# Kernel optimization log

Measured on AMD Instinct MI355X. Metric: run time of the kernel, lower is better.

Reference implementation:

```python
import jax, jax.numpy as jnp
import numpy as np

B, T, H = 256, 512, 1024


def setup_inputs() -> dict:
    key = jax.random.key(0)
    ks = jax.random.split(key, 11)
    s = 1.0 / np.sqrt(H)
    u = lambda k, shape: jax.random.uniform(k, shape, jnp.float32, -s, s)
    return {
        "x": jax.random.normal(ks[0], (B, T), jnp.float32),
        "W_ih1": u(ks[1], (4 * H, 1)),
        "W_hh1": u(ks[2], (4 * H, H)),
        "b_ih1": u(ks[3], (4 * H,)),
        "b_hh1": u(ks[4], (4 * H,)),
        "W_ih2": u(ks[5], (4 * H, H)),
        "W_hh2": u(ks[6], (4 * H, H)),
        "b_ih2": u(ks[7], (4 * H,)),
        "b_hh2": u(ks[8], (4 * H,)),
        "W_out": u(ks[9], (1, H)),
        "b_out": u(ks[10], (1,)),
        "future": 0,
    }


def _lstm_cell(x, h, c, W_ih, W_hh, b):
    # PyTorch LSTMCell gate order: i, f, g, o
    gates = x @ W_ih.T + h @ W_hh.T + b
    i, f, g, o = jnp.split(gates, 4, axis=-1)
    c_new = jax.nn.sigmoid(f) * c + jax.nn.sigmoid(i) * jnp.tanh(g)
    h_new = jax.nn.sigmoid(o) * jnp.tanh(c_new)
    return h_new, c_new


def reference(x, W_ih1, W_hh1, b_ih1, b_hh1, W_ih2, W_hh2, b_ih2, b_hh2, W_out, b_out, future):
    Bn = x.shape[0]
    Hd = W_hh1.shape[1]
    b1 = b_ih1 + b_hh1
    b2 = b_ih2 + b_hh2

    def step(carry, x_t):
        h1, c1, h2, c2 = carry
        h1, c1 = _lstm_cell(x_t, h1, c1, W_ih1, W_hh1, b1)
        h2, c2 = _lstm_cell(h1, h2, c2, W_ih2, W_hh2, b2)
        out = h2 @ W_out.T + b_out  # [B, 1]
        return (h1, c1, h2, c2), out

    xs = x.T[:, :, None]  # [T, B, 1]
    carry0 = tuple(jnp.zeros((Bn, Hd), x.dtype) for _ in range(4))
    carry, outs = jax.lax.scan(step, carry0, xs)  # outs: [T, B, 1]
    outputs = [outs[:, :, 0].T]  # [B, T]

    # closed-loop future prediction (future is a static Python int)
    out = outs[-1]
    for _ in range(future):
        carry, out = step(carry, out)
        outputs.append(out)
    return jnp.concatenate(outputs, axis=1)
```

## Files before the change

### kernel.cpp

```cpp
#include <hip/hip_runtime.h>
#include <hip/hip_cooperative_groups.h>
#include <math.h>

namespace cg = cooperative_groups;

#define Bsz 256
#define Tsz 512
#define GSTR 258

using half8 = __attribute__((ext_vector_type(8))) _Float16;
using half4 = __attribute__((ext_vector_type(4))) _Float16;
using f32x4 = __attribute__((ext_vector_type(4))) float;

#define MFMA_V(acc, a, b) (acc) = __builtin_amdgcn_mfma_f32_16x16x32_f16((a), (b), (acc), 0, 0, 0)
#define INV2048 (1.0f / 2048.0f)

__device__ __forceinline__ float sigm(float v)   { return 1.0f / (1.0f + expf(-v)); }
__device__ __forceinline__ float tanh_f(float v) { float e = expf(2.0f * v); return 1.0f - 2.0f / (e + 1.0f); }

__device__ __forceinline__ void split8(const float* p, half8& hi, half8& lo) {
    float4 v0 = *(const float4*)p, v1 = *(const float4*)(p + 4);
    float vv[8] = {v0.x, v0.y, v0.z, v0.w, v1.x, v1.y, v1.z, v1.w};
    #pragma unroll
    for (int j = 0; j < 8; ++j) {
        hi[j] = (_Float16)vv[j];
        lo[j] = (_Float16)((vv[j] - (float)hi[j]) * 2048.0f);
    }
}

__device__ __forceinline__ void step_barrier(unsigned* bar0, unsigned* bar1,
                                             unsigned* phase2, unsigned* dummyv,
                                             int bx, int isLead, unsigned xcc,
                                             unsigned nLead, unsigned it1) {
    __syncthreads();
    if (threadIdx.x == 0) {
        unsigned old = __hip_atomic_fetch_add(&bar0[(bx & 15) << 5], 1u,
                                              __ATOMIC_RELAXED, __HIP_MEMORY_SCOPE_AGENT);
        if ((old & 15u) == 15u)
            __hip_atomic_fetch_add(bar1, 1u, __ATOMIC_RELAXED, __HIP_MEMORY_SCOPE_AGENT);
        if (isLead) {
            while (__hip_atomic_load(bar1, __ATOMIC_RELAXED, __HIP_MEMORY_SCOPE_AGENT) < 16u * it1)
                __builtin_amdgcn_s_sleep(1);
            __hip_atomic_fetch_add(&dummyv[xcc << 5], 1u,
                                   __ATOMIC_ACQ_REL, __HIP_MEMORY_SCOPE_AGENT);
            __hip_atomic_fetch_add(phase2, 1u,
                                   __ATOMIC_RELAXED, __HIP_MEMORY_SCOPE_AGENT);
        }
        while (__hip_atomic_load(phase2, __ATOMIC_RELAXED, __HIP_MEMORY_SCOPE_AGENT) < nLead * it1)
            __builtin_amdgcn_s_sleep(1);
        asm volatile("buffer_inv sc0" ::: "memory");
    }
    __syncthreads();
}

__global__ __launch_bounds__(512, 1) void lstm_persist(
    const float* __restrict__ x,
    const float* __restrict__ W_ih1, const float* __restrict__ W_hh1,
    const float* __restrict__ b_ih1, const float* __restrict__ b_hh1,
    const float* __restrict__ W_ih2, const float* __restrict__ W_hh2,
    const float* __restrict__ b_ih2, const float* __restrict__ b_hh2,
    const float* __restrict__ W_out, const float* __restrict__ b_out,
    float* __restrict__ out, char* __restrict__ ws)
{
    __shared__ float gAcc[32 * GSTR];
    __shared__ float poArr[2 * GSTR];
    __shared__ float bp[32], wihp[32], woutp[8];
    __shared__ float bouts_s;
    __shared__ unsigned isLead_s, xcc_s, nLead_s;

    cg::grid_group grid = cg::this_grid();

    const int tid  = threadIdx.x;
    const int lane = tid & 63;
    const int wv   = tid >> 6;
    const int m    = lane & 15;
    const int quad = lane >> 4;
    const int bx   = blockIdx.x;
    const bool isL2 = (bx >= 128);
    const int rg   = isL2 ? (bx - 128) : bx;
    const int HO   = rg << 3;

    float*    xT       = (float*)ws;
    _Float16* hswz     = (_Float16*)(ws + (512 << 10));
    float*    partials = (float*)(ws + (512 << 10) + (4 << 20));
    unsigned* bar0     = (unsigned*)(ws + (512 << 10) + (4 << 20) + (256 << 10));
    unsigned* bar1     = bar0 + 1024;
    unsigned* phase2   = bar0 + 1056;
    unsigned* nLeadCt  = bar0 + 1057;
    unsigned* claimA   = bar0 + 1088;
    unsigned* dummyv   = bar0 + 1536;

    #define HBUF(p, l, hl) (hswz + ((((p) << 2) | ((l) << 1) | (hl)) << 18))

    if (bx == 0)
        for (int i = tid; i < 2048; i += 512) bar0[i] = 0u;
    if (tid < 32) {
        const int row = ((tid & 3) << 10) + HO + (tid >> 2);
        if (!isL2) {
            bp[tid]   = b_ih1[row] + b_hh1[row];
            wihp[tid] = W_ih1[row];
        } else {
            bp[tid] = b_ih2[row] + b_hh2[row];
            if (tid < 8) woutp[tid] = W_out[HO + tid];
        }
        if (tid == 0) bouts_s = b_out[0];
    }
    {
        const int gidx = bx * 512 + tid;
        *(float4*)((char*)hswz + (2u << 20) + (size_t)gidx * 16) = make_float4(0, 0, 0, 0);
        xT[gidx] = x[(gidx & 255) * Tsz + (gidx >> 8)];
    }

    grid.sync();

    if (tid == 0) {
        unsigned xcc;
        asm volatile("s_getreg_b32 %0, hwreg(HW_REG_XCC_ID)" : "=s"(xcc));
        xcc &= 7u;
        xcc_s = xcc;
        unsigned old = __hip_atomic_fetch_add(&claimA[xcc << 5], 1u,
                                              __ATOMIC_RELAXED, __HIP_MEMORY_SCOPE_AGENT);
        isLead_s = (old == 0u);
        if (old == 0u)
            __hip_atomic_fetch_add(nLeadCt, 1u,
                                   __ATOMIC_RELAXED, __HIP_MEMORY_SCOPE_AGENT);
    }
    grid.sync();
    if (tid == 0)
        nLead_s = __hip_atomic_load(nLeadCt, __ATOMIC_RELAXED, __HIP_MEMORY_SCOPE_AGENT);
    __syncthreads();
    const int      isLead = (int)isLead_s;
    const unsigned xcc    = xcc_s;
    const unsigned nLead  = nLead_s;

    const int b_ep = tid & 255, hg = tid >> 8;
    const int k0e  = HO + (hg << 2);
    const int wofs = ((b_ep >> 4) << 14) + ((k0e >> 5) << 9)
                   + (((b_ep & 15) | (((k0e >> 3) & 3) << 4)) << 3) + (k0e & 7);

    if (!isL2) {
        half8 wh[2][4], wl[2][4];
        #pragma unroll
        for (int mt = 0; mt < 2; ++mt) {
            const int pr = (mt << 4) + m;
            const size_t rw = (size_t)(((pr & 3) << 10) + HO + (pr >> 2)) << 10;
            #pragma unroll
            for (int kt = 0; kt < 4; ++kt) {
                const int k = (wv << 7) + (kt << 5) + (quad << 3);
                split8(W_hh1 + rw + k, wh[mt][kt], wl[mt][kt]);
            }
        }
        for (int idx = tid; idx < 8192; idx += 512) {
            const int p = idx >> 8, b = idx & 255;
            gAcc[p * GSTR + b] = bp[p] + xT[b] * wihp[p];
        }
        __syncthreads();
        float cr[4] = {0, 0, 0, 0};

        for (int it = 0; it <= Tsz; ++it) {
            const int parW = it & 1;
            const int parR = parW ^ 1;

            float xnext = 0.0f;
            if (it + 1 < Tsz) xnext = xT[((it + 1) << 8) + b_ep];

            if (wv == 0 && it >= 2) {
                const float* pp = partials + (parW << 15) + (bx << 7);
                float s = pp[lane] + pp[lane + 64];
                s += __shfl_xor(s, 32); s += __shfl_xor(s, 16); s += __shfl_xor(s, 8);
                s += __shfl_xor(s, 4);  s += __shfl_xor(s, 2);  s += __shfl_xor(s, 1);
                if (lane == 0) out[(bx << 9) + (it - 2)] = bouts_s + s;
            }

            if (it < Tsz) {
                const _Float16* bhB = HBUF(parR, 0, 0);
                const _Float16* blB = HBUF(parR, 0, 1);
                const int lo_off = (wv << 11) + (lane << 3);
                #pragma unroll 2
                for (int bi = 0; bi < 16; ++bi) {
                    const int btl = (bi + (wv << 1)) & 15;
                    const _Float16* ph = bhB + (btl << 14) + lo_off;
                    const _Float16* pl = blB + (btl << 14) + lo_off;
                    f32x4 a0[2] = {(f32x4){0,0,0,0}, (f32x4){0,0,0,0}};
                    f32x4 a1[2] = {(f32x4){0,0,0,0}, (f32x4){0,0,0,0}};
                    half8 bh = *(const half8*)ph;
                    half8 bl = *(const half8*)pl;
                    #pragma unroll
                    for (int kt = 0; kt < 4; ++kt) {
                        half8 bhN, blN;
                        if (kt < 3) {
                            bhN = *(const half8*)(ph + ((kt + 1) << 9));
                            blN = *(const half8*)(pl + ((kt + 1) << 9));
                        }
                        MFMA_V(a0[0], wh[0][kt], bh);
                        MFMA_V(a1[0], wh[0][kt], bl);
                        MFMA_V(a1[0], wl[0][kt], bh);
                        MFMA_V(a0[1], wh[1][kt], bh);
                        MFMA_V(a1[1], wh[1][kt], bl);
                        MFMA_V(a1[1], wl[1][kt], bh);
                        bh = bhN; bl = blN;
                    }
                    const int col = (btl << 4) + m;
                    #pragma unroll
                    for (int mt = 0; mt < 2; ++mt)
                        #pragma unroll
                        for (int r = 0; r < 4; ++r)
                            atomicAdd(&gAcc[((mt << 4) + (quad << 2) + r) * GSTR + col],
                                      a0[mt][r] + a1[mt][r] * INV2048);
                }
            }

            __syncthreads();

            if (it < Tsz) {
                half4 hhi, hlo;
                #pragma unroll
                for (int j = 0; j < 4; ++j) {
                    const int p = (hg << 4) + (j << 2);
                    const float gi = gAcc[(p + 0) * GSTR + b_ep];
                    const float gf = gAcc[(p + 1) * GSTR + b_ep];
                    const float gg = gAcc[(p + 2) * GSTR + b_ep];
                    const float go = gAcc[(p + 3) * GSTR + b_ep];
                    const float c  = sigm(gf) * cr[j] + sigm(gi) * tanh_f(gg);
                    cr[j] = c;
                    const float hn = sigm(go) * tanh_f(c);
                    hhi[j] = (_Float16)hn;
                    hlo[j] = (_Float16)((hn - (float)hhi[j]) * 2048.0f);
                }
                *(half4*)(HBUF(parW, 0, 0) + wofs) = hhi;
                *(half4*)(HBUF(parW, 0, 1) + wofs) = hlo;
                if (it + 1 < Tsz) {
                    #pragma unroll
                    for (int p = (hg << 4); p < (hg << 4) + 16; ++p)
                        gAcc[p * GSTR + b_ep] = bp[p] + xnext * wihp[p];
                }
            }

            step_barrier(bar0, bar1, phase2, dummyv, bx, isLead, xcc, nLead,
                         (unsigned)(it + 1));
        }
    } else {
        half8 wh[2][8], wl[2][8];
        #pragma unroll
        for (int mt = 0; mt < 2; ++mt) {
            const int pr = (mt << 4) + m;
            const size_t rw = (size_t)(((pr & 3) << 10) + HO + (pr >> 2)) << 10;
            #pragma unroll
            for (int kt = 0; kt < 8; ++kt) {
                const int k = (wv << 8) + (kt << 5) + (quad << 3);
                const float* p = (k < 1024) ? (W_ih2 + rw + k)
                                            : (W_hh2 + rw + k - 1024);
                split8(p, wh[mt][kt], wl[mt][kt]);
            }
        }
        for (int idx = tid; idx < 8192; idx += 512) {
            const int p = idx >> 8, b = idx & 255;
            gAcc[p * GSTR + b] = bp[p];
        }
        __syncthreads();
        float cr[4] = {0, 0, 0, 0};

        for (int it = 0; it <= Tsz; ++it) {
            const int parW = it & 1;
            const int parR = parW ^ 1;

            if (wv == 0 && it >= 2) {
                const float* pp = partials + (parW << 15) + (bx << 7);
                float s = pp[lane] + pp[lane + 64];
                s += __shfl_xor(s, 32); s += __shfl_xor(s, 16); s += __shfl_xor(s, 8);
                s += __shfl_xor(s, 4);  s += __shfl_xor(s, 2);  s += __shfl_xor(s, 1);
                if (lane == 0) out[(bx << 9) + (it - 2)] = bouts_s + s;
            }

            if (it >= 1) {
                const bool hi2 = (wv >= 4);
                const _Float16* bhB = hi2 ? HBUF(parW, 1, 0) : HBUF(parR, 0, 0);
                const _Float16* blB = hi2 ? HBUF(parW, 1, 1) : HBUF(parR, 0, 1);
                const int lo_off = ((wv & 3) << 12) + (lane << 3);
                #pragma unroll 2
                for (int bi = 0; bi < 16; ++bi) {
                    const int btl = (bi + (wv << 1)) & 15;
                    const _Float16* ph = bhB + (btl << 14) + lo_off;
                    const _Float16* pl = blB + (btl << 14) + lo_off;
                    f32x4 a0[2] = {(f32x4){0,0,0,0}, (f32x4){0,0,0,0}};
                    f32x4 a1[2] = {(f32x4){0,0,0,0}, (f32x4){0,0,0,0}};
                    half8 bh = *(const half8*)ph;
                    half8 bl = *(const half8*)pl;
                    #pragma unroll
                    for (int kt = 0; kt < 8; ++kt) {
                        half8 bhN, blN;
                        if (kt < 7) {
                            bhN = *(const half8*)(ph + ((kt + 1) << 9));
                            blN = *(const half8*)(pl + ((kt + 1) << 9));
                        }
                        MFMA_V(a0[0], wh[0][kt], bh);
                        MFMA_V(a1[0], wh[0][kt], bl);
                        MFMA_V(a1[0], wl[0][kt], bh);
                        MFMA_V(a0[1], wh[1][kt], bh);
                        MFMA_V(a1[1], wh[1][kt], bl);
                        MFMA_V(a1[1], wl[1][kt], bh);
                        bh = bhN; bl = blN;
                    }
                    const int col = (btl << 4) + m;
                    #pragma unroll
                    for (int mt = 0; mt < 2; ++mt)
                        #pragma unroll
                        for (int r = 0; r < 4; ++r)
                            atomicAdd(&gAcc[((mt << 4) + (quad << 2) + r) * GSTR + col],
                                      a0[mt][r] + a1[mt][r] * INV2048);
                }
            }

            __syncthreads();

            if (it >= 1) {
                half4 hhi, hlo;
                float po = 0.0f;
                #pragma unroll
                for (int j = 0; j < 4; ++j) {
                    const int p = (hg << 4) + (j << 2);
                    const float gi = gAcc[(p + 0) * GSTR + b_ep];
                    const float gf = gAcc[(p + 1) * GSTR + b_ep];
                    const float gg = gAcc[(p + 2) * GSTR + b_ep];
                    const float go = gAcc[(p + 3) * GSTR + b_ep];
                    const float c  = sigm(gf) * cr[j] + sigm(gi) * tanh_f(gg);
                    cr[j] = c;
                    const float hn = sigm(go) * tanh_f(c);
                    hhi[j] = (_Float16)hn;
                    hlo[j] = (_Float16)((hn - (float)hhi[j]) * 2048.0f);
                    po += hn * woutp[(hg << 2) + j];
                }
                *(half4*)(HBUF(parR, 1, 0) + wofs) = hhi;
                *(half4*)(HBUF(parR, 1, 1) + wofs) = hlo;
                poArr[hg * GSTR + b_ep] = po;
                #pragma unroll
                for (int p = (hg << 4); p < (hg << 4) + 16; ++p)
                    gAcc[p * GSTR + b_ep] = bp[p];
            }
            __syncthreads();
            if (it >= 1 && tid < 256) {
                const float s = poArr[tid] + poArr[GSTR + tid];
                partials[(parR << 15) + (tid << 7) + rg] = s;
            }

            step_barrier(bar0, bar1, phase2, dummyv, bx, isLead, xcc, nLead,
                         (unsigned)(it + 1));
        }
    }

    if (wv == 0) {
        const float* pp = partials + (1 << 15) + (bx << 7);
        float s = pp[lane] + pp[lane + 64];
        s += __shfl_xor(s, 32); s += __shfl_xor(s, 16); s += __shfl_xor(s, 8);
        s += __shfl_xor(s, 4);  s += __shfl_xor(s, 2);  s += __shfl_xor(s, 1);
        if (lane == 0) out[(bx << 9) + (Tsz - 1)] = bouts_s + s;
    }
    #undef HBUF
}

extern "C" void kernel_launch(void* const* d_in, const int* in_sizes, int n_in,
                              void* d_out, int out_size, void* d_ws, size_t ws_size,
                              hipStream_t stream)
{
    const float* x     = (const float*)d_in[0];
    const float* W_ih1 = (const float*)d_in[1];
    const float* W_hh1 = (const float*)d_in[2];
    const float* b_ih1 = (const float*)d_in[3];
    const float* b_hh1 = (const float*)d_in[4];
    const float* W_ih2 = (const float*)d_in[5];
    const float* W_hh2 = (const float*)d_in[6];
    const float* b_ih2 = (const float*)d_in[7];
    const float* b_hh2 = (const float*)d_in[8];
    const float* W_out = (const float*)d_in[9];
    const float* b_out = (const float*)d_in[10];
    float* out = (float*)d_out;
    char*  ws  = (char*)d_ws;

    void* args[] = {
        (void*)&x,
        (void*)&W_ih1, (void*)&W_hh1, (void*)&b_ih1, (void*)&b_hh1,
        (void*)&W_ih2, (void*)&W_hh2, (void*)&b_ih2, (void*)&b_hh2,
        (void*)&W_out, (void*)&b_out, (void*)&out, (void*)&ws,
    };
    hipLaunchCooperativeKernel((const void*)lstm_persist,
                               dim3(256), dim3(512), args, 0, stream);
}
```

Baseline: 47.48 ms.

## Use 4-slot hidden-state ring and full cross-XCC barrier only every fourth step

Grows the hidden-state and partial-sum buffers from double to quadruple buffering. The barrier now runs the expensive leader/phase2 cross-XCC handshake with its acquire-release fence only every fourth step; other steps spin on the arrival counter alone. Hidden-state and partial stores become relaxed agent-scope atomic stores so they bypass non-coherent caches without a fence each step. The aim is to cut per-timestep global synchronisation cost. The risk is a subtle memory-ordering bug, since visibility across XCCs now relies on atomic stores plus buffer_inv rather than a release fence.

Result: faster. 46.12 ms (-2.9%).

```diff
diff --git a/kernel.cpp b/kernel.cpp
--- a/kernel.cpp
+++ b/kernel.cpp
@@ -26,6 +26,16 @@
         hi[j] = (_Float16)vv[j];
         lo[j] = (_Float16)((vv[j] - (float)hi[j]) * 2048.0f);
     }
+}
+
+__device__ __forceinline__ void st_h4(_Float16* p, half4 v) {
+    unsigned long long u;
+    __builtin_memcpy(&u, &v, 8);
+    __hip_atomic_store((unsigned long long*)(void*)p, u,
+                       __ATOMIC_RELAXED, __HIP_MEMORY_SCOPE_AGENT);
+}
+__device__ __forceinline__ void st_f(float* p, float v) {
+    __hip_atomic_store(p, v, __ATOMIC_RELAXED, __HIP_MEMORY_SCOPE_AGENT);
 }
 
 __device__ __forceinline__ void step_barrier(unsigned* bar0, unsigned* bar1,
@@ -38,16 +48,22 @@
                                               __ATOMIC_RELAXED, __HIP_MEMORY_SCOPE_AGENT);
         if ((old & 15u) == 15u)
             __hip_atomic_fetch_add(bar1, 1u, __ATOMIC_RELAXED, __HIP_MEMORY_SCOPE_AGENT);
-        if (isLead) {
+        const bool l2i = (it1 & 3u) == 0u;
+        if (l2i) {
+            if (isLead) {
+                while (__hip_atomic_load(bar1, __ATOMIC_RELAXED, __HIP_MEMORY_SCOPE_AGENT) < 16u * it1)
+                    __builtin_amdgcn_s_sleep(1);
+                __hip_atomic_fetch_add(&dummyv[xcc << 5], 1u,
+                                       __ATOMIC_ACQ_REL, __HIP_MEMORY_SCOPE_AGENT);
+                __hip_atomic_fetch_add(phase2, 1u,
+                                       __ATOMIC_RELAXED, __HIP_MEMORY_SCOPE_AGENT);
+            }
+            while (__hip_atomic_load(phase2, __ATOMIC_RELAXED, __HIP_MEMORY_SCOPE_AGENT) < nLead * (it1 >> 2))
+                __builtin_amdgcn_s_sleep(1);
+        } else {
             while (__hip_atomic_load(bar1, __ATOMIC_RELAXED, __HIP_MEMORY_SCOPE_AGENT) < 16u * it1)
                 __builtin_amdgcn_s_sleep(1);
-            __hip_atomic_fetch_add(&dummyv[xcc << 5], 1u,
-                                   __ATOMIC_ACQ_REL, __HIP_MEMORY_SCOPE_AGENT);
-            __hip_atomic_fetch_add(phase2, 1u,
-                                   __ATOMIC_RELAXED, __HIP_MEMORY_SCOPE_AGENT);
-        }
-        while (__hip_atomic_load(phase2, __ATOMIC_RELAXED, __HIP_MEMORY_SCOPE_AGENT) < nLead * it1)
-            __builtin_amdgcn_s_sleep(1);
+        }
         asm volatile("buffer_inv sc0" ::: "memory");
     }
     __syncthreads();
@@ -82,8 +98,8 @@
 
     float*    xT       = (float*)ws;
     _Float16* hswz     = (_Float16*)(ws + (512 << 10));
-    float*    partials = (float*)(ws + (512 << 10) + (4 << 20));
-    unsigned* bar0     = (unsigned*)(ws + (512 << 10) + (4 << 20) + (256 << 10));
+    float*    partials = (float*)(ws + (512 << 10) + (8 << 20));
+    unsigned* bar0     = (unsigned*)(ws + (512 << 10) + (8 << 20) + (512 << 10));
     unsigned* bar1     = bar0 + 1024;
     unsigned* phase2   = bar0 + 1056;
     unsigned* nLeadCt  = bar0 + 1057;
@@ -107,7 +123,7 @@
     }
     {
         const int gidx = bx * 512 + tid;
-        *(float4*)((char*)hswz + (2u << 20) + (size_t)gidx * 16) = make_float4(0, 0, 0, 0);
+        *(float4*)((char*)hswz + (6u << 20) + (size_t)gidx * 16) = make_float4(0, 0, 0, 0);
         xT[gidx] = x[(gidx & 255) * Tsz + (gidx >> 8)];
     }
 
@@ -158,23 +174,24 @@
         float cr[4] = {0, 0, 0, 0};
 
         for (int it = 0; it <= Tsz; ++it) {
-            const int parW = it & 1;
-            const int parR = parW ^ 1;
+            const int sW = it & 3;
+            const int sR = (it + 3) & 3;
+            const int sP = it & 3;
 
             float xnext = 0.0f;
             if (it + 1 < Tsz) xnext = xT[((it + 1) << 8) + b_ep];
 
             if (wv == 0 && it >= 2) {
-                const float* pp = partials + (parW << 15) + (bx << 7);
+                const float* pp = partials + (sP << 15) + (bx << 7);
                 float s = pp[lane] + pp[lane + 64];
                 s += __shfl_xor(s, 32); s += __shfl_xor(s, 16); s += __shfl_xor(s, 8);
                 s += __shfl_xor(s, 4);  s += __shfl_xor(s, 2);  s += __shfl_xor(s, 1);
-                if (lane == 0) out[(bx << 9) + (it - 2)] = bouts_s + s;
+                if (lane == 0) st_f(&out[(bx << 9) + (it - 2)], bouts_s + s);
             }
 
             if (it < Tsz) {
-                const _Float16* bhB = HBUF(parR, 0, 0);
-                const _Float16* blB = HBUF(parR, 0, 1);
+                const _Float16* bhB = HBUF(sR, 0, 0);
+                const _Float16* blB = HBUF(sR, 0, 1);
                 const int lo_off = (wv << 11) + (lane << 3);
                 #pragma unroll 2
                 for (int bi = 0; bi < 16; ++bi) {
@@ -227,8 +244,8 @@
                     hhi[j] = (_Float16)hn;
                     hlo[j] = (_Float16)((hn - (float)hhi[j]) * 2048.0f);
                 }
-                *(half4*)(HBUF(parW, 0, 0) + wofs) = hhi;
-                *(half4*)(HBUF(parW, 0, 1) + wofs) = hlo;
+                st_h4(HBUF(sW, 0, 0) + wofs, hhi);
+                st_h4(HBUF(sW, 0, 1) + wofs, hlo);
                 if (it + 1 < Tsz) {
                     #pragma unroll
                     for (int p = (hg << 4); p < (hg << 4) + 16; ++p)
@@ -261,21 +278,24 @@
         float cr[4] = {0, 0, 0, 0};
 
         for (int it = 0; it <= Tsz; ++it) {
-            const int parW = it & 1;
-            const int parR = parW ^ 1;
+            const int sR1 = (it + 3) & 3;
+            const int sW2 = (it + 3) & 3;
+            const int sR2 = (it + 2) & 3;
+            const int sP  = it & 3;
+            const int sPW = (it + 1) & 3;
 
             if (wv == 0 && it >= 2) {
-                const float* pp = partials + (parW << 15) + (bx << 7);
+                const float* pp = partials + (sP << 15) + (bx << 7);
                 float s = pp[lane] + pp[lane + 64];
                 s += __shfl_xor(s, 32); s += __shfl_xor(s, 16); s += __shfl_xor(s, 8);
                 s += __shfl_xor(s, 4);  s += __shfl_xor(s, 2);  s += __shfl_xor(s, 1);
-                if (lane == 0) out[(bx << 9) + (it - 2)] = bouts_s + s;
+                if (lane == 0) st_f(&out[(bx << 9) + (it - 2)], bouts_s + s);
             }
 
             if (it >= 1) {
                 const bool hi2 = (wv >= 4);
-                const _Float16* bhB = hi2 ? HBUF(parW, 1, 0) : HBUF(parR, 0, 0);
-                const _Float16* blB = hi2 ? HBUF(parW, 1, 1) : HBUF(parR, 0, 1);
+                const _Float16* bhB = hi2 ? HBUF(sR2, 1, 0) : HBUF(sR1, 0, 0);
+                const _Float16* blB = hi2 ? HBUF(sR2, 1, 1) : HBUF(sR1, 0, 1);
                 const int lo_off = ((wv & 3) << 12) + (lane << 3);
                 #pragma unroll 2
                 for (int bi = 0; bi < 16; ++bi) {
@@ -330,8 +350,8 @@
                     hlo[j] = (_Float16)((hn - (float)hhi[j]) * 2048.0f);
                     po += hn * woutp[(hg << 2) + j];
                 }
-                *(half4*)(HBUF(parR, 1, 0) + wofs) = hhi;
-                *(half4*)(HBUF(parR, 1, 1) + wofs) = hlo;
+                st_h4(HBUF(sW2, 1, 0) + wofs, hhi);
+                st_h4(HBUF(sW2, 1, 1) + wofs, hlo);
                 poArr[hg * GSTR + b_ep] = po;
                 #pragma unroll
                 for (int p = (hg << 4); p < (hg << 4) + 16; ++p)
@@ -340,7 +360,7 @@
             __syncthreads();
             if (it >= 1 && tid < 256) {
                 const float s = poArr[tid] + poArr[GSTR + tid];
-                partials[(parR << 15) + (tid << 7) + rg] = s;
+                st_f(&partials[(sPW << 15) + (tid << 7) + rg], s);
             }
 
             step_barrier(bar0, bar1, phase2, dummyv, bx, isLead, xcc, nLead,
@@ -353,7 +373,7 @@
         float s = pp[lane] + pp[lane + 64];
         s += __shfl_xor(s, 32); s += __shfl_xor(s, 16); s += __shfl_xor(s, 8);
         s += __shfl_xor(s, 4);  s += __shfl_xor(s, 2);  s += __shfl_xor(s, 1);
-        if (lane == 0) out[(bx << 9) + (Tsz - 1)] = bouts_s + s;
+        if (lane == 0) st_f(&out[(bx << 9) + (Tsz - 1)], bouts_s + s);
     }
     #undef HBUF
 }
```
